# Optimization experiments

Measured on AMD Instinct MI355X. Metric: run time of the kernel, lower is better.

## Reference

```python
import jax, jax.numpy as jnp
import numpy as np

N, E = 20000, 320000
ATOM_IN, BOND_IN, HIDDEN, LAYERS = 64, 16, 256, 5
BN_EPS = 1e-5


def setup_inputs() -> dict:
    key = jax.random.key(0)
    ks = jax.random.split(key, 16)
    s = 0.05
    return {
        "x": jax.random.normal(ks[0], (N, ATOM_IN), jnp.float32),
        "edge_attr": jax.random.normal(ks[1], (E, BOND_IN), jnp.float32),
        "edge_index": jax.random.randint(ks[2], (2, E), 0, N, jnp.int32),
        "Wa": jax.random.normal(ks[3], (ATOM_IN, HIDDEN), jnp.float32) * s,
        "ba": jnp.zeros((HIDDEN,), jnp.float32),
        "We": jax.random.normal(ks[4], (BOND_IN, HIDDEN), jnp.float32) * s,
        "be": jnp.zeros((HIDDEN,), jnp.float32),
        "eps": jnp.zeros((LAYERS,), jnp.float32),  # train_eps=True, init 0
        "W1": jax.random.normal(ks[5], (LAYERS, HIDDEN, HIDDEN), jnp.float32) * s,
        "b1": jnp.zeros((LAYERS, HIDDEN), jnp.float32),
        "W2": jax.random.normal(ks[6], (LAYERS, HIDDEN, HIDDEN), jnp.float32) * s,
        "b2": jnp.zeros((LAYERS, HIDDEN), jnp.float32),
        "gamma": jnp.ones((LAYERS, HIDDEN), jnp.float32),
        "beta": jnp.zeros((LAYERS, HIDDEN), jnp.float32),
    }


def reference(x, edge_attr, edge_index, Wa, ba, We, be, eps, W1, b1, W2, b2, gamma, beta):
    src, dst = edge_index[0], edge_index[1]  # messages flow src -> dst (PyG x_j = x[src])
    h = x @ Wa + ba                          # [N, H] atom_proj
    e = edge_attr @ We + be                  # [E, H] edge_proj
    for l in range(LAYERS):
        # GINEConv: aggr = sum_j relu(x_j + e_ij); out = mlp((1+eps)*x_i + aggr)
        msg = jax.nn.relu(h[src] + e)                              # [E, H]
        aggr = jax.ops.segment_sum(msg, dst, num_segments=N)        # [N, H]
        z = (1.0 + eps[l]) * h + aggr
        z = jax.nn.relu(z @ W1[l] + b1[l]) @ W2[l] + b2[l]          # 2-layer MLP
        # BatchNorm1d over the node dimension (batch statistics)
        mu = jnp.mean(z, axis=0)
        var = jnp.var(z, axis=0)
        z = (z - mu) * jax.lax.rsqrt(var + BN_EPS) * gamma[l] + beta[l]
        z = jax.nn.relu(z)
        # dropout is identity in deterministic reference (eval)
        h = h + z  # residual
    return h
```

## Files before the change

kernel.cpp:

```cpp
#include <hip/hip_runtime.h>

typedef unsigned short u16;
typedef __attribute__((ext_vector_type(4))) float f32x4;
typedef __attribute__((ext_vector_type(8))) short s16x8;
typedef __attribute__((ext_vector_type(8))) unsigned short u16x8;
typedef __attribute__((ext_vector_type(4))) unsigned short u16x4;

__device__ inline float bf2f(u16 u) {
    unsigned v = ((unsigned)u) << 16;
    return __builtin_bit_cast(float, v);
}
__device__ inline u16 f2bf(float f) {
    unsigned u = __builtin_bit_cast(unsigned, f);
    unsigned r = (u + 0x7FFFu + ((u >> 16) & 1u)) >> 16;
    return (u16)r;
}

__global__ void count_kernel(const int* __restrict__ dst, int E, int* __restrict__ counts) {
    int e = blockIdx.x * 256 + threadIdx.x;
    if (e < E) atomicAdd(&counts[dst[e]], 1);
}

__global__ __launch_bounds__(1024) void scan_kernel(const int* __restrict__ counts,
    int* __restrict__ row_start, int* __restrict__ cursor, int NN) {
    __shared__ int sh[1024];
    const int tid = threadIdx.x;
    const int CH = (NN + 1023) / 1024;
    const int base = tid * CH;
    int sum = 0;
    for (int i = 0; i < CH; ++i) { int idx = base + i; if (idx < NN) sum += counts[idx]; }
    sh[tid] = sum; __syncthreads();
    for (int off = 1; off < 1024; off <<= 1) {
        int v = (tid >= off) ? sh[tid - off] : 0;
        __syncthreads();
        sh[tid] += v;
        __syncthreads();
    }
    int run = sh[tid] - sum;
    for (int i = 0; i < CH; ++i) {
        int idx = base + i;
        if (idx <= NN) {
            row_start[idx] = run;
            if (idx < NN) { cursor[idx] = run; run += counts[idx]; }
        }
    }
}

__global__ void pos_kernel(const int* __restrict__ src, const int* __restrict__ dst, int E,
    int* __restrict__ cursor, int* __restrict__ pos, int* __restrict__ src_perm) {
    int e = blockIdx.x * 256 + threadIdx.x;
    if (e < E) {
        int p = atomicAdd(&cursor[dst[e]], 1);
        pos[e] = p;
        src_perm[p] = src[e];
    }
}

__global__ void prep_kernel(const float* __restrict__ x, const float* __restrict__ Wa,
    const float* __restrict__ We, const float* __restrict__ W1, const float* __restrict__ W2,
    u16* __restrict__ x_bf, u16* __restrict__ Wat, u16* __restrict__ Wet,
    u16* __restrict__ W1t, u16* __restrict__ W2t, int NN) {
    int i = blockIdx.x * 256 + threadIdx.x;
    const int S0 = NN * 16;
    if (i < S0) {
        f32x4 v = *(const f32x4*)(x + (size_t)i * 4);
        u16x4 o; o.x = f2bf(v[0]); o.y = f2bf(v[1]); o.z = f2bf(v[2]); o.w = f2bf(v[3]);
        *(u16x4*)(x_bf + (size_t)i * 4) = o;
        return;
    }
    i -= S0;
    if (i < 16384) { int n = i >> 6, k = i & 63; Wat[i] = f2bf(Wa[k * 256 + n]); return; }
    i -= 16384;
    if (i < 8192) { int n = i >> 5, k = i & 31; Wet[i] = f2bf(k < 16 ? We[k * 256 + n] : 0.f); return; }
    i -= 8192;
    if (i < 327680) { int l = i >> 16, r = i & 65535, n = r >> 8, k = r & 255;
        W1t[i] = f2bf(W1[(size_t)l * 65536 + k * 256 + n]); return; }
    i -= 327680;
    if (i < 327680) { int l = i >> 16, r = i & 65535, n = r >> 8, k = r & 255;
        W2t[i] = f2bf(W2[(size_t)l * 65536 + k * 256 + n]); return; }
}

__global__ void permute_pad_eattr_kernel(const float* __restrict__ ea, const int* __restrict__ pos,
                                         int E, u16* __restrict__ out) {
    int e = blockIdx.x * 256 + threadIdx.x;
    if (e >= E) return;
    const float* r = ea + (size_t)e * 16;
    f32x4 q0 = *(const f32x4*)(r + 0);
    f32x4 q1 = *(const f32x4*)(r + 4);
    f32x4 q2 = *(const f32x4*)(r + 8);
    f32x4 q3 = *(const f32x4*)(r + 12);
    u16x8 v0, v1, z;
#pragma unroll
    for (int j = 0; j < 4; ++j) {
        v0[j] = f2bf(q0[j]); v0[4 + j] = f2bf(q1[j]);
        v1[j] = f2bf(q2[j]); v1[4 + j] = f2bf(q3[j]);
        z[j] = 0; z[4 + j] = 0;
    }
    u16* o = out + (size_t)pos[e] * 32;
    *(u16x8*)(o + 0) = v0;
    *(u16x8*)(o + 8) = v1;
    *(u16x8*)(o + 16) = z;
    *(u16x8*)(o + 24) = z;
}

template <bool WF32, bool WB16>
__global__ __launch_bounds__(256) void gemm_kernel(
    const u16* __restrict__ A, int lda, int M,
    const u16* __restrict__ Bt, int K,
    const float* __restrict__ bias,
    float* __restrict__ outF, u16* __restrict__ outB, int ldo) {
    __shared__ u16 As[128 * 32];
    __shared__ u16 Bs[128 * 32];
    const int tid = threadIdx.x, lane = tid & 63, wave = tid >> 6;
    const int m0 = blockIdx.x * 128, n0 = blockIdx.y * 128;
    const int wr = (wave >> 1) * 64, wc = (wave & 1) * 64;

    const f32x4 zero4 = {0.f, 0.f, 0.f, 0.f};
    f32x4 acc[4][4];
#pragma unroll
    for (int m = 0; m < 4; ++m)
#pragma unroll
        for (int n = 0; n < 4; ++n) acc[m][n] = zero4;

    for (int k0 = 0; k0 < K; k0 += 32) {
#pragma unroll
        for (int i = 0; i < 2; ++i) {
            int seg = i * 256 + tid;
            int row = seg >> 2, sk = seg & 3;
            int gr = m0 + row; gr = gr < M ? gr : M - 1;
            u16x8 va = *(const u16x8*)(A + (size_t)gr * lda + k0 + sk * 8);
            *(u16x8*)(&As[row * 32 + sk * 8]) = va;
            u16x8 vb = *(const u16x8*)(Bt + (size_t)(n0 + row) * K + k0 + sk * 8);
            *(u16x8*)(&Bs[row * 32 + sk * 8]) = vb;
        }
        __syncthreads();
        const int rsel = lane & 15, koff = (lane >> 4) * 8;
        s16x8 af[4], bf[4];
#pragma unroll
        for (int m = 0; m < 4; ++m) af[m] = *(const s16x8*)(&As[(wr + m * 16 + rsel) * 32 + koff]);
#pragma unroll
        for (int n = 0; n < 4; ++n) bf[n] = *(const s16x8*)(&Bs[(wc + n * 16 + rsel) * 32 + koff]);
#pragma unroll
        for (int m = 0; m < 4; ++m)
#pragma unroll
            for (int n = 0; n < 4; ++n)
                acc[m][n] = __builtin_amdgcn_mfma_f32_16x16x32_bf16(af[m], bf[n], acc[m][n], 0, 0, 0);
        __syncthreads();
    }

    const int cl = lane & 15, rq = lane >> 4;
#pragma unroll
    for (int n = 0; n < 4; ++n) {
        const int gcol = n0 + wc + n * 16 + cl;
        const float bv = bias[gcol];
#pragma unroll
        for (int m = 0; m < 4; ++m) {
#pragma unroll
            for (int j = 0; j < 4; ++j) {
                int grow = m0 + wr + m * 16 + rq * 4 + j;
                if (grow < M) {
                    float v = acc[m][n][j] + bv;
                    long orow = (long)grow;
                    if constexpr (WF32) outF[orow * ldo + gcol] = v;
                    if constexpr (WB16) outB[orow * ldo + gcol] = f2bf(v);
                }
            }
        }
    }
}

__global__ __launch_bounds__(256) void mlp_fused_kernel(
    const u16* __restrict__ z, int M,
    const u16* __restrict__ W1t, const float* __restrict__ b1,
    const u16* __restrict__ W2t, const float* __restrict__ b2,
    u16* __restrict__ y2,
    float* __restrict__ colsum, float* __restrict__ colsumsq) {
    __shared__ u16 As[64 * 32];
    __shared__ u16 Bs[256 * 32];
    __shared__ u16 Ys[64 * 260];
    const int tid = threadIdx.x, lane = tid & 63, wave = tid >> 6;
    const int m0 = blockIdx.x * 64;
    const int wc = wave * 64;
    const int rsel = lane & 15, koff = (lane >> 4) * 8;
    const int cl = lane & 15, rq = lane >> 4;

    const f32x4 zero4 = {0.f, 0.f, 0.f, 0.f};
    f32x4 acc[4][4];
#pragma unroll
    for (int m = 0; m < 4; ++m)
#pragma unroll
        for (int n = 0; n < 4; ++n) acc[m][n] = zero4;

    for (int k0 = 0; k0 < 256; k0 += 32) {
        {
            int row = tid >> 2, sk = tid & 3;
            int gr = m0 + row; gr = gr < M ? gr : M - 1;
            u16x8 va = *(const u16x8*)(z + (size_t)gr * 256 + k0 + sk * 8);
            *(u16x8*)(&As[row * 32 + sk * 8]) = va;
        }
#pragma unroll
        for (int i = 0; i < 4; ++i) {
            int seg = i * 256 + tid;
            int row = seg >> 2, sk = seg & 3;
            u16x8 vb = *(const u16x8*)(W1t + (size_t)row * 256 + k0 + sk * 8);
            *(u16x8*)(&Bs[row * 32 + sk * 8]) = vb;
        }
        __syncthreads();
        s16x8 af[4], bf[4];
#pragma unroll
        for (int m = 0; m < 4; ++m) af[m] = *(const s16x8*)(&As[(m * 16 + rsel) * 32 + koff]);
#pragma unroll
        for (int n = 0; n < 4; ++n) bf[n] = *(const s16x8*)(&Bs[(wc + n * 16 + rsel) * 32 + koff]);
#pragma unroll
        for (int m = 0; m < 4; ++m)
#pragma unroll
            for (int n = 0; n < 4; ++n)
                acc[m][n] = __builtin_amdgcn_mfma_f32_16x16x32_bf16(af[m], bf[n], acc[m][n], 0, 0, 0);
        __syncthreads();
    }
#pragma unroll
    for (int n = 0; n < 4; ++n) {
        const int gcol = wc + n * 16 + cl;
        const float bv = b1[gcol];
#pragma unroll
        for (int m = 0; m < 4; ++m) {
#pragma unroll
            for (int j = 0; j < 4; ++j) {
                int row = m * 16 + rq * 4 + j;
                float v = fmaxf(acc[m][n][j] + bv, 0.f);
                Ys[row * 260 + gcol] = f2bf(v);
            }
        }
        acc[0][n] = zero4; acc[1][n] = zero4; acc[2][n] = zero4; acc[3][n] = zero4;
    }

    for (int k0 = 0; k0 < 256; k0 += 32) {
#pragma unroll
        for (int i = 0; i < 4; ++i) {
            int seg = i * 256 + tid;
            int row = seg >> 2, sk = seg & 3;
            u16x8 vb = *(const u16x8*)(W2t + (size_t)row * 256 + k0 + sk * 8);
            *(u16x8*)(&Bs[row * 32 + sk * 8]) = vb;
        }
        __syncthreads();
        s16x8 af[4], bf[4];
#pragma unroll
        for (int m = 0; m < 4; ++m) af[m] = *(const s16x8*)(&Ys[(m * 16 + rsel) * 260 + k0 + koff]);
#pragma unroll
        for (int n = 0; n < 4; ++n) bf[n] = *(const s16x8*)(&Bs[(wc + n * 16 + rsel) * 32 + koff]);
#pragma unroll
        for (int m = 0; m < 4; ++m)
#pragma unroll
            for (int n = 0; n < 4; ++n)
                acc[m][n] = __builtin_amdgcn_mfma_f32_16x16x32_bf16(af[m], bf[n], acc[m][n], 0, 0, 0);
        __syncthreads();
    }
#pragma unroll
    for (int n = 0; n < 4; ++n) {
        const int gcol = wc + n * 16 + cl;
        const float bv = b2[gcol];
        float s = 0.f, ss = 0.f;
#pragma unroll
        for (int m = 0; m < 4; ++m) {
#pragma unroll
            for (int j = 0; j < 4; ++j) {
                int grow = m0 + m * 16 + rq * 4 + j;
                if (grow < M) {
                    float v = acc[m][n][j] + bv;
                    y2[(size_t)grow * 256 + gcol] = f2bf(v);
                    s += v; ss += v * v;
                }
            }
        }
        s += __shfl_down(s, 32); ss += __shfl_down(ss, 32);
        s += __shfl_down(s, 16); ss += __shfl_down(ss, 16);
        if (rq == 0) {
            atomicAdd(&colsum[gcol], s);
            atomicAdd(&colsumsq[gcol], ss);
        }
    }
}

__global__ __launch_bounds__(256) void agg_kernel(
    const int* __restrict__ row_start, const int* __restrict__ src_perm,
    const u16* __restrict__ e_perm, const u16* __restrict__ h_bf,
    const float* __restrict__ h, const float* __restrict__ eps, int layer,
    u16* __restrict__ z_bf, int NN) {
    const int node = blockIdx.x * 4 + (threadIdx.x >> 6);
    const int lane = threadIdx.x & 63;
    const int c0 = lane * 4;
    if (node >= NN) return;
    const int s0 = row_start[node], s1 = row_start[node + 1];
    float a0 = 0.f, a1 = 0.f, a2 = 0.f, a3 = 0.f;
    const u16* ep = e_perm + (size_t)s0 * 256 + c0;
    int k = s0;
    for (; k + 1 < s1; k += 2, ep += 512) {
        const int sa = src_perm[k];
        const int sb = src_perm[k + 1];
        u16x4 ha = *(const u16x4*)(h_bf + (size_t)sa * 256 + c0);
        u16x4 hb = *(const u16x4*)(h_bf + (size_t)sb * 256 + c0);
        u16x4 ea = *(const u16x4*)(ep);
        u16x4 eb = *(const u16x4*)(ep + 256);
        a0 += fmaxf(bf2f(ha.x) + bf2f(ea.x), 0.f);
        a1 += fmaxf(bf2f(ha.y) + bf2f(ea.y), 0.f);
        a2 += fmaxf(bf2f(ha.z) + bf2f(ea.z), 0.f);
        a3 += fmaxf(bf2f(ha.w) + bf2f(ea.w), 0.f);
        a0 += fmaxf(bf2f(hb.x) + bf2f(eb.x), 0.f);
        a1 += fmaxf(bf2f(hb.y) + bf2f(eb.y), 0.f);
        a2 += fmaxf(bf2f(hb.z) + bf2f(eb.z), 0.f);
        a3 += fmaxf(bf2f(hb.w) + bf2f(eb.w), 0.f);
    }
    if (k < s1) {
        const int sa = src_perm[k];
        u16x4 ha = *(const u16x4*)(h_bf + (size_t)sa * 256 + c0);
        u16x4 ea = *(const u16x4*)(ep);
        a0 += fmaxf(bf2f(ha.x) + bf2f(ea.x), 0.f);
        a1 += fmaxf(bf2f(ha.y) + bf2f(ea.y), 0.f);
        a2 += fmaxf(bf2f(ha.z) + bf2f(ea.z), 0.f);
        a3 += fmaxf(bf2f(ha.w) + bf2f(ea.w), 0.f);
    }
    const float c = 1.f + eps[layer];
    const f32x4 hr = *(const f32x4*)(h + (size_t)node * 256 + c0);
    u16x4 z;
    z.x = f2bf(c * hr[0] + a0); z.y = f2bf(c * hr[1] + a1);
    z.z = f2bf(c * hr[2] + a2); z.w = f2bf(c * hr[3] + a3);
    *(u16x4*)(z_bf + (size_t)node * 256 + c0) = z;
}

__global__ __launch_bounds__(256) void bn_res_kernel(
    const u16* __restrict__ y2, const float* __restrict__ colsum,
    const float* __restrict__ colsumsq, const float* __restrict__ gamma,
    const float* __restrict__ beta, const float* __restrict__ hin,
    float* __restrict__ hout, u16* __restrict__ h_bf, int write_bf,
    float invN, int total4) {
    const int i = blockIdx.x * 256 + threadIdx.x;
    if (i >= total4) return;
    const size_t base = (size_t)i * 4;
    const int c0 = (int)(base & 255);
    u16x4 yv = *(const u16x4*)(y2 + base);
    f32x4 hv = *(const f32x4*)(hin + base);
    u16 ys[4] = {yv.x, yv.y, yv.z, yv.w};
    f32x4 res;
#pragma unroll
    for (int j = 0; j < 4; ++j) {
        const int c = c0 + j;
        const float mu = colsum[c] * invN;
        const float var = colsumsq[c] * invN - mu * mu;
        const float sc = gamma[c] * rsqrtf(var + 1e-5f);
        const float sh = beta[c] - mu * sc;
        float v = bf2f(ys[j]) * sc + sh;
        v = fmaxf(v, 0.f);
        res[j] = hv[j] + v;
    }
    *(f32x4*)(hout + base) = res;
    if (write_bf) {
        u16x4 hb; hb.x = f2bf(res[0]); hb.y = f2bf(res[1]); hb.z = f2bf(res[2]); hb.w = f2bf(res[3]);
        *(u16x4*)(h_bf + base) = hb;
    }
}

extern "C" void kernel_launch(void* const* d_in, const int* in_sizes, int n_in,
                              void* d_out, int out_size, void* d_ws, size_t ws_size,
                              hipStream_t stream) {
    const float* x    = (const float*)d_in[0];
    const float* ea   = (const float*)d_in[1];
    const int*   ei   = (const int*)d_in[2];
    const float* Wa   = (const float*)d_in[3];
    const float* ba   = (const float*)d_in[4];
    const float* We   = (const float*)d_in[5];
    const float* be   = (const float*)d_in[6];
    const float* eps  = (const float*)d_in[7];
    const float* W1   = (const float*)d_in[8];
    const float* b1   = (const float*)d_in[9];
    const float* W2   = (const float*)d_in[10];
    const float* b2   = (const float*)d_in[11];
    const float* gamma= (const float*)d_in[12];
    const float* beta = (const float*)d_in[13];

    const int NN = in_sizes[0] / 64;
    const int EE = in_sizes[1] / 16;
    const int* src = ei;
    const int* dst = ei + EE;

    char* p = (char*)d_ws;
    auto alloc = [&](size_t bytes) -> char* {
        char* r = p;
        p += (bytes + 255) & ~(size_t)255;
        return r;
    };
    int*   counts   = (int*)alloc((size_t)(NN + 1) * 4);
    float* colsum   = (float*)alloc(5 * 256 * 4);
    float* colsumsq = (float*)alloc(5 * 256 * 4);
    size_t zbytes   = (size_t)(p - (char*)counts);
    int*   row_start= (int*)alloc((size_t)(NN + 1) * 4);
    int*   cursor   = (int*)alloc((size_t)NN * 4);
    int*   pos      = (int*)alloc((size_t)EE * 4);
    int*   src_perm = (int*)alloc((size_t)EE * 4);
    u16*   x_bf     = (u16*)alloc((size_t)NN * 64 * 2);
    u16*   Wat      = (u16*)alloc(256 * 64 * 2);
    u16*   Wet      = (u16*)alloc(256 * 32 * 2);
    u16*   W1t      = (u16*)alloc((size_t)5 * 65536 * 2);
    u16*   W2t      = (u16*)alloc((size_t)5 * 65536 * 2);
    u16*   eap_perm = (u16*)alloc((size_t)EE * 32 * 2);
    u16*   e_perm   = (u16*)alloc((size_t)EE * 256 * 2);
    float* h        = (float*)alloc((size_t)NN * 256 * 4);
    u16*   h_bf     = (u16*)alloc((size_t)NN * 256 * 2);
    u16*   z_bf     = (u16*)alloc((size_t)NN * 256 * 2);
    u16*   y2       = (u16*)alloc((size_t)NN * 256 * 2);

    hipMemsetAsync(counts, 0, zbytes, stream);

    const int eb = (EE + 255) / 256;
    count_kernel<<<eb, 256, 0, stream>>>(dst, EE, counts);
    scan_kernel<<<1, 1024, 0, stream>>>(counts, row_start, cursor, NN);
    pos_kernel<<<eb, 256, 0, stream>>>(src, dst, EE, cursor, pos, src_perm);

    const int prep_total = NN * 16 + 16384 + 8192 + 327680 + 327680;
    prep_kernel<<<(prep_total + 255) / 256, 256, 0, stream>>>(x, Wa, We, W1, W2, x_bf, Wat, Wet, W1t, W2t, NN);
    permute_pad_eattr_kernel<<<eb, 256, 0, stream>>>(ea, pos, EE, eap_perm);

    dim3 gh((NN + 127) / 128, 2);
    gemm_kernel<true, true><<<gh, 256, 0, stream>>>(
        x_bf, 64, NN, Wat, 64, ba, h, h_bf, 256);
    dim3 ge((EE + 127) / 128, 2);
    gemm_kernel<false, true><<<ge, 256, 0, stream>>>(
        eap_perm, 32, EE, Wet, 32, be, nullptr, e_perm, 256);

    const float invN = 1.f / (float)NN;
    const int nb4 = (NN * 64 + 255) / 256;
    const int mlp_blocks = (NN + 63) / 64;
    for (int l = 0; l < 5; ++l) {
        agg_kernel<<<(NN + 3) / 4, 256, 0, stream>>>(
            row_start, src_perm, e_perm, h_bf, h, eps, l, z_bf, NN);
        mlp_fused_kernel<<<mlp_blocks, 256, 0, stream>>>(
            z_bf, NN, W1t + (size_t)l * 65536, b1 + l * 256,
            W2t + (size_t)l * 65536, b2 + l * 256, y2,
            colsum + l * 256, colsumsq + l * 256);
        bn_res_kernel<<<nb4, 256, 0, stream>>>(
            y2, colsum + l * 256, colsumsq + l * 256, gamma + l * 256, beta + l * 256,
            h, (l == 4) ? (float*)d_out : h, h_bf, (l < 4) ? 1 : 0, invN, NN * 64);
    }
}
```

Measured before the change: 692.7 us.

## Coalesce GEMM epilogue stores via LDS staging and widen aggregation loads

The edge-projection GEMM and the fused MLP kernel now stage bf16 outputs in shared memory and write full 16-byte rows to global memory, replacing scattered 2-byte stores. The aggregation kernel now has each half-wave handle a separate edge with 8-channel (16-byte) loads, four edges per iteration, and combines the halves with a cross-lane shuffle. This targets store inefficiency in the large edge GEMM and adds memory-level parallelism to the gather. In exchange it uses extra LDS, adds a barrier, and does masked dummy loads for tail edges.

After: 621.5 us. 1.11x faster.

```diff
diff --git a/kernel.cpp b/kernel.cpp
--- a/kernel.cpp
+++ b/kernel.cpp
@@ -103,8 +103,7 @@
     *(u16x8*)(o + 24) = z;
 }
 
-template <bool WF32, bool WB16>
-__global__ __launch_bounds__(256) void gemm_kernel(
+__global__ __launch_bounds__(256) void gemm_h0_kernel(
     const u16* __restrict__ A, int lda, int M,
     const u16* __restrict__ Bt, int K,
     const float* __restrict__ bias,
@@ -160,11 +159,81 @@
                 int grow = m0 + wr + m * 16 + rq * 4 + j;
                 if (grow < M) {
                     float v = acc[m][n][j] + bv;
-                    long orow = (long)grow;
-                    if constexpr (WF32) outF[orow * ldo + gcol] = v;
-                    if constexpr (WB16) outB[orow * ldo + gcol] = f2bf(v);
+                    outF[(size_t)grow * ldo + gcol] = v;
+                    outB[(size_t)grow * ldo + gcol] = f2bf(v);
                 }
             }
+        }
+    }
+}
+
+__global__ __launch_bounds__(256) void gemm_coal_kernel(
+    const u16* __restrict__ A, int lda, int M,
+    const u16* __restrict__ Bt, int K,
+    const float* __restrict__ bias,
+    u16* __restrict__ outB, int ldo) {
+    __shared__ u16 As[128 * 32];
+    __shared__ u16 Bs[128 * 32];
+    __shared__ u16 Cs[128 * 136];
+    const int tid = threadIdx.x, lane = tid & 63, wave = tid >> 6;
+    const int m0 = blockIdx.x * 128, n0 = blockIdx.y * 128;
+    const int wr = (wave >> 1) * 64, wc = (wave & 1) * 64;
+
+    const f32x4 zero4 = {0.f, 0.f, 0.f, 0.f};
+    f32x4 acc[4][4];
+#pragma unroll
+    for (int m = 0; m < 4; ++m)
+#pragma unroll
+        for (int n = 0; n < 4; ++n) acc[m][n] = zero4;
+
+    for (int k0 = 0; k0 < K; k0 += 32) {
+#pragma unroll
+        for (int i = 0; i < 2; ++i) {
+            int seg = i * 256 + tid;
+            int row = seg >> 2, sk = seg & 3;
+            int gr = m0 + row; gr = gr < M ? gr : M - 1;
+            u16x8 va = *(const u16x8*)(A + (size_t)gr * lda + k0 + sk * 8);
+            *(u16x8*)(&As[row * 32 + sk * 8]) = va;
+            u16x8 vb = *(const u16x8*)(Bt + (size_t)(n0 + row) * K + k0 + sk * 8);
+            *(u16x8*)(&Bs[row * 32 + sk * 8]) = vb;
+        }
+        __syncthreads();
+        const int rsel = lane & 15, koff = (lane >> 4) * 8;
+        s16x8 af[4], bf[4];
+#pragma unroll
+        for (int m = 0; m < 4; ++m) af[m] = *(const s16x8*)(&As[(wr + m * 16 + rsel) * 32 + koff]);
+#pragma unroll
+        for (int n = 0; n < 4; ++n) bf[n] = *(const s16x8*)(&Bs[(wc + n * 16 + rsel) * 32 + koff]);
+#pragma unroll
+        for (int m = 0; m < 4; ++m)
+#pragma unroll
+            for (int n = 0; n < 4; ++n)
+                acc[m][n] = __builtin_amdgcn_mfma_f32_16x16x32_bf16(af[m], bf[n], acc[m][n], 0, 0, 0);
+        __syncthreads();
+    }
+
+    const int cl = lane & 15, rq = lane >> 4;
+#pragma unroll
+    for (int n = 0; n < 4; ++n) {
+        const int col = wc + n * 16 + cl;
+        const float bv = bias[n0 + col];
+#pragma unroll
+        for (int m = 0; m < 4; ++m) {
+#pragma unroll
+            for (int j = 0; j < 4; ++j) {
+                int row = wr + m * 16 + rq * 4 + j;
+                Cs[row * 136 + col] = f2bf(acc[m][n][j] + bv);
+            }
+        }
+    }
+    __syncthreads();
+    for (int r0 = 0; r0 < 128; r0 += 16) {
+        int row = r0 + (tid >> 4);
+        int gr = m0 + row;
+        int cc = (tid & 15) * 8;
+        if (gr < M) {
+            u16x8 v = *(u16x8*)(&Cs[row * 136 + cc]);
+            *(u16x8*)(outB + (size_t)gr * ldo + n0 + cc) = v;
         }
     }
 }
@@ -264,12 +333,10 @@
         for (int m = 0; m < 4; ++m) {
 #pragma unroll
             for (int j = 0; j < 4; ++j) {
-                int grow = m0 + m * 16 + rq * 4 + j;
-                if (grow < M) {
-                    float v = acc[m][n][j] + bv;
-                    y2[(size_t)grow * 256 + gcol] = f2bf(v);
-                    s += v; ss += v * v;
-                }
+                int row = m * 16 + rq * 4 + j;
+                float v = acc[m][n][j] + bv;
+                Ys[row * 260 + gcol] = f2bf(v);
+                if (m0 + row < M) { s += v; ss += v * v; }
             }
         }
         s += __shfl_down(s, 32); ss += __shfl_down(ss, 32);
@@ -278,6 +345,13 @@
             atomicAdd(&colsum[gcol], s);
             atomicAdd(&colsumsq[gcol], ss);
         }
+    }
+    __syncthreads();
+    for (int r0 = 0; r0 < 64; r0 += 8) {
+        int row = r0 + (tid >> 5);
+        int gr = m0 + row;
+        int cc = (tid & 31) * 8;
+        if (gr < M) *(u16x8*)(y2 + (size_t)gr * 256 + cc) = *(u16x8*)(&Ys[row * 260 + cc]);
     }
 }
 
@@ -288,43 +362,44 @@
     u16* __restrict__ z_bf, int NN) {
     const int node = blockIdx.x * 4 + (threadIdx.x >> 6);
     const int lane = threadIdx.x & 63;
-    const int c0 = lane * 4;
+    const int half = lane >> 5;
+    const int c0 = (lane & 31) * 8;
     if (node >= NN) return;
     const int s0 = row_start[node], s1 = row_start[node + 1];
-    float a0 = 0.f, a1 = 0.f, a2 = 0.f, a3 = 0.f;
-    const u16* ep = e_perm + (size_t)s0 * 256 + c0;
-    int k = s0;
-    for (; k + 1 < s1; k += 2, ep += 512) {
-        const int sa = src_perm[k];
-        const int sb = src_perm[k + 1];
-        u16x4 ha = *(const u16x4*)(h_bf + (size_t)sa * 256 + c0);
-        u16x4 hb = *(const u16x4*)(h_bf + (size_t)sb * 256 + c0);
-        u16x4 ea = *(const u16x4*)(ep);
-        u16x4 eb = *(const u16x4*)(ep + 256);
-        a0 += fmaxf(bf2f(ha.x) + bf2f(ea.x), 0.f);
-        a1 += fmaxf(bf2f(ha.y) + bf2f(ea.y), 0.f);
-        a2 += fmaxf(bf2f(ha.z) + bf2f(ea.z), 0.f);
-        a3 += fmaxf(bf2f(ha.w) + bf2f(ea.w), 0.f);
-        a0 += fmaxf(bf2f(hb.x) + bf2f(eb.x), 0.f);
-        a1 += fmaxf(bf2f(hb.y) + bf2f(eb.y), 0.f);
-        a2 += fmaxf(bf2f(hb.z) + bf2f(eb.z), 0.f);
-        a3 += fmaxf(bf2f(hb.w) + bf2f(eb.w), 0.f);
-    }
-    if (k < s1) {
-        const int sa = src_perm[k];
-        u16x4 ha = *(const u16x4*)(h_bf + (size_t)sa * 256 + c0);
-        u16x4 ea = *(const u16x4*)(ep);
-        a0 += fmaxf(bf2f(ha.x) + bf2f(ea.x), 0.f);
-        a1 += fmaxf(bf2f(ha.y) + bf2f(ea.y), 0.f);
-        a2 += fmaxf(bf2f(ha.z) + bf2f(ea.z), 0.f);
-        a3 += fmaxf(bf2f(ha.w) + bf2f(ea.w), 0.f);
-    }
-    const float c = 1.f + eps[layer];
-    const f32x4 hr = *(const f32x4*)(h + (size_t)node * 256 + c0);
-    u16x4 z;
-    z.x = f2bf(c * hr[0] + a0); z.y = f2bf(c * hr[1] + a1);
-    z.z = f2bf(c * hr[2] + a2); z.w = f2bf(c * hr[3] + a3);
-    *(u16x4*)(z_bf + (size_t)node * 256 + c0) = z;
+    float a[8] = {0.f, 0.f, 0.f, 0.f, 0.f, 0.f, 0.f, 0.f};
+    for (int k = s0; k < s1; k += 4) {
+        const int ke0 = k + half, ke1 = k + 2 + half;
+        const bool v0 = ke0 < s1, v1 = ke1 < s1;
+        const int i0 = v0 ? ke0 : s1 - 1;
+        const int i1 = v1 ? ke1 : s1 - 1;
+        const int su0 = src_perm[i0];
+        const int su1 = src_perm[i1];
+        u16x8 e0 = *(const u16x8*)(e_perm + (size_t)i0 * 256 + c0);
+        u16x8 h0 = *(const u16x8*)(h_bf + (size_t)su0 * 256 + c0);
+        u16x8 e1 = *(const u16x8*)(e_perm + (size_t)i1 * 256 + c0);
+        u16x8 h1 = *(const u16x8*)(h_bf + (size_t)su1 * 256 + c0);
+        const float m0 = v0 ? 1.f : 0.f;
+        const float m1 = v1 ? 1.f : 0.f;
+#pragma unroll
+        for (int j = 0; j < 8; ++j) {
+            a[j] += m0 * fmaxf(bf2f((u16)e0[j]) + bf2f((u16)h0[j]), 0.f);
+            a[j] += m1 * fmaxf(bf2f((u16)e1[j]) + bf2f((u16)h1[j]), 0.f);
+        }
+    }
+#pragma unroll
+    for (int j = 0; j < 8; ++j) a[j] += __shfl_xor(a[j], 32);
+    if (half == 0) {
+        const float c = 1.f + eps[layer];
+        const f32x4 hr0 = *(const f32x4*)(h + (size_t)node * 256 + c0);
+        const f32x4 hr1 = *(const f32x4*)(h + (size_t)node * 256 + c0 + 4);
+        u16x8 z;
+#pragma unroll
+        for (int j = 0; j < 4; ++j) {
+            z[j] = f2bf(c * hr0[j] + a[j]);
+            z[4 + j] = f2bf(c * hr1[j] + a[4 + j]);
+        }
+        *(u16x8*)(z_bf + (size_t)node * 256 + c0) = z;
+    }
 }
 
 __global__ __launch_bounds__(256) void bn_res_kernel(
@@ -420,11 +495,11 @@
     permute_pad_eattr_kernel<<<eb, 256, 0, stream>>>(ea, pos, EE, eap_perm);
 
     dim3 gh((NN + 127) / 128, 2);
-    gemm_kernel<true, true><<<gh, 256, 0, stream>>>(
+    gemm_h0_kernel<<<gh, 256, 0, stream>>>(
         x_bf, 64, NN, Wat, 64, ba, h, h_bf, 256);
     dim3 ge((EE + 127) / 128, 2);
-    gemm_kernel<false, true><<<ge, 256, 0, stream>>>(
-        eap_perm, 32, EE, Wet, 32, be, nullptr, e_perm, 256);
+    gemm_coal_kernel<<<ge, 256, 0, stream>>>(
+        eap_perm, 32, EE, Wet, 32, be, e_perm, 256);
 
     const float invN = 1.f / (float)NN;
     const int nb4 = (NN * 64 + 255) / 256;
```

## Recompute edge projection on the fly inside aggregation via MFMA instead of materializing

Applied to the files above, without the earlier changes.

Drops the precomputed E×256 bf16 edge-embedding buffer and its GEMM. The aggregation kernel now recomputes each edge's projection per layer with MFMA from the padded 32-wide edge attributes, with the bias folded in as a constant-1 column, and adds the gathered source node features. This removes a large per-layer read of edge embeddings and one write pass, at the cost of redundant MFMA compute each layer and a cross-lane reduction. The MLP epilogue is also changed to stage outputs through shared memory for coalesced vector stores.

Result: slower. 862.8 us (+24.6%).

```diff
diff --git a/kernel.cpp b/kernel.cpp
--- a/kernel.cpp
+++ b/kernel.cpp
@@ -57,7 +57,8 @@
 }
 
 __global__ void prep_kernel(const float* __restrict__ x, const float* __restrict__ Wa,
-    const float* __restrict__ We, const float* __restrict__ W1, const float* __restrict__ W2,
+    const float* __restrict__ We, const float* __restrict__ be,
+    const float* __restrict__ W1, const float* __restrict__ W2,
     u16* __restrict__ x_bf, u16* __restrict__ Wat, u16* __restrict__ Wet,
     u16* __restrict__ W1t, u16* __restrict__ W2t, int NN) {
     int i = blockIdx.x * 256 + threadIdx.x;
@@ -71,7 +72,11 @@
     i -= S0;
     if (i < 16384) { int n = i >> 6, k = i & 63; Wat[i] = f2bf(Wa[k * 256 + n]); return; }
     i -= 16384;
-    if (i < 8192) { int n = i >> 5, k = i & 31; Wet[i] = f2bf(k < 16 ? We[k * 256 + n] : 0.f); return; }
+    if (i < 8192) {
+        int n = i >> 5, k = i & 31;
+        float v = (k < 16) ? We[k * 256 + n] : ((k == 16) ? be[n] : 0.f);
+        Wet[i] = f2bf(v); return;
+    }
     i -= 8192;
     if (i < 327680) { int l = i >> 16, r = i & 65535, n = r >> 8, k = r & 255;
         W1t[i] = f2bf(W1[(size_t)l * 65536 + k * 256 + n]); return; }
@@ -89,22 +94,22 @@
     f32x4 q1 = *(const f32x4*)(r + 4);
     f32x4 q2 = *(const f32x4*)(r + 8);
     f32x4 q3 = *(const f32x4*)(r + 12);
-    u16x8 v0, v1, z;
+    u16x8 v0, v1, m, z;
 #pragma unroll
     for (int j = 0; j < 4; ++j) {
         v0[j] = f2bf(q0[j]); v0[4 + j] = f2bf(q1[j]);
         v1[j] = f2bf(q2[j]); v1[4 + j] = f2bf(q3[j]);
-        z[j] = 0; z[4 + j] = 0;
-    }
+        m[j] = 0; m[4 + j] = 0; z[j] = 0; z[4 + j] = 0;
+    }
+    m[0] = 0x3F80;
     u16* o = out + (size_t)pos[e] * 32;
     *(u16x8*)(o + 0) = v0;
     *(u16x8*)(o + 8) = v1;
-    *(u16x8*)(o + 16) = z;
+    *(u16x8*)(o + 16) = m;
     *(u16x8*)(o + 24) = z;
 }
 
-template <bool WF32, bool WB16>
-__global__ __launch_bounds__(256) void gemm_kernel(
+__global__ __launch_bounds__(256) void gemm_h0_kernel(
     const u16* __restrict__ A, int lda, int M,
     const u16* __restrict__ Bt, int K,
     const float* __restrict__ bias,
@@ -160,9 +165,8 @@
                 int grow = m0 + wr + m * 16 + rq * 4 + j;
                 if (grow < M) {
                     float v = acc[m][n][j] + bv;
-                    long orow = (long)grow;
-                    if constexpr (WF32) outF[orow * ldo + gcol] = v;
-                    if constexpr (WB16) outB[orow * ldo + gcol] = f2bf(v);
+                    outF[(size_t)grow * ldo + gcol] = v;
+                    outB[(size_t)grow * ldo + gcol] = f2bf(v);
                 }
             }
         }
@@ -264,12 +268,10 @@
         for (int m = 0; m < 4; ++m) {
 #pragma unroll
             for (int j = 0; j < 4; ++j) {
-                int grow = m0 + m * 16 + rq * 4 + j;
-                if (grow < M) {
-                    float v = acc[m][n][j] + bv;
-                    y2[(size_t)grow * 256 + gcol] = f2bf(v);
-                    s += v; ss += v * v;
-                }
+                int row = m * 16 + rq * 4 + j;
+                float v = acc[m][n][j] + bv;
+                Ys[row * 260 + gcol] = f2bf(v);
+                if (m0 + row < M) { s += v; ss += v * v; }
             }
         }
         s += __shfl_down(s, 32); ss += __shfl_down(ss, 32);
@@ -279,52 +281,88 @@
             atomicAdd(&colsumsq[gcol], ss);
         }
     }
-}
-
-__global__ __launch_bounds__(256) void agg_kernel(
+    __syncthreads();
+    for (int r0 = 0; r0 < 64; r0 += 8) {
+        int row = r0 + (tid >> 5);
+        int gr = m0 + row;
+        int cc = (tid & 31) * 8;
+        if (gr < M) *(u16x8*)(y2 + (size_t)gr * 256 + cc) = *(u16x8*)(&Ys[row * 260 + cc]);
+    }
+}
+
+__global__ __launch_bounds__(256) void agg_mfma_kernel(
     const int* __restrict__ row_start, const int* __restrict__ src_perm,
-    const u16* __restrict__ e_perm, const u16* __restrict__ h_bf,
-    const float* __restrict__ h, const float* __restrict__ eps, int layer,
+    const u16* __restrict__ eap, const u16* __restrict__ Wet,
+    const u16* __restrict__ h_bf, const float* __restrict__ h,
+    const float* __restrict__ eps, int layer,
     u16* __restrict__ z_bf, int NN) {
-    const int node = blockIdx.x * 4 + (threadIdx.x >> 6);
-    const int lane = threadIdx.x & 63;
-    const int c0 = lane * 4;
+    __shared__ u16 WetL[16 * 64 * 8];
+    const int tid = threadIdx.x;
+    const int lane = tid & 63;
+    const int rsel = lane & 15;
+    const int q = lane >> 4;
+#pragma unroll
+    for (int i = 0; i < 4; ++i) {
+        int ent = tid + i * 256;
+        int b = ent >> 6, l = ent & 63;
+        int row = b * 16 + (l & 15);
+        int ko = (l >> 4) * 8;
+        *(u16x8*)(&WetL[ent * 8]) = *(const u16x8*)(Wet + row * 32 + ko);
+    }
+    __syncthreads();
+
+    const int node = blockIdx.x * 4 + (tid >> 6);
     if (node >= NN) return;
     const int s0 = row_start[node], s1 = row_start[node + 1];
-    float a0 = 0.f, a1 = 0.f, a2 = 0.f, a3 = 0.f;
-    const u16* ep = e_perm + (size_t)s0 * 256 + c0;
-    int k = s0;
-    for (; k + 1 < s1; k += 2, ep += 512) {
-        const int sa = src_perm[k];
-        const int sb = src_perm[k + 1];
-        u16x4 ha = *(const u16x4*)(h_bf + (size_t)sa * 256 + c0);
-        u16x4 hb = *(const u16x4*)(h_bf + (size_t)sb * 256 + c0);
-        u16x4 ea = *(const u16x4*)(ep);
-        u16x4 eb = *(const u16x4*)(ep + 256);
-        a0 += fmaxf(bf2f(ha.x) + bf2f(ea.x), 0.f);
-        a1 += fmaxf(bf2f(ha.y) + bf2f(ea.y), 0.f);
-        a2 += fmaxf(bf2f(ha.z) + bf2f(ea.z), 0.f);
-        a3 += fmaxf(bf2f(ha.w) + bf2f(ea.w), 0.f);
-        a0 += fmaxf(bf2f(hb.x) + bf2f(eb.x), 0.f);
-        a1 += fmaxf(bf2f(hb.y) + bf2f(eb.y), 0.f);
-        a2 += fmaxf(bf2f(hb.z) + bf2f(eb.z), 0.f);
-        a3 += fmaxf(bf2f(hb.w) + bf2f(eb.w), 0.f);
-    }
-    if (k < s1) {
-        const int sa = src_perm[k];
-        u16x4 ha = *(const u16x4*)(h_bf + (size_t)sa * 256 + c0);
-        u16x4 ea = *(const u16x4*)(ep);
-        a0 += fmaxf(bf2f(ha.x) + bf2f(ea.x), 0.f);
-        a1 += fmaxf(bf2f(ha.y) + bf2f(ea.y), 0.f);
-        a2 += fmaxf(bf2f(ha.z) + bf2f(ea.z), 0.f);
-        a3 += fmaxf(bf2f(ha.w) + bf2f(ea.w), 0.f);
-    }
+
+    const f32x4 zero4 = {0.f, 0.f, 0.f, 0.f};
+    f32x4 sums[16];
+#pragma unroll
+    for (int b = 0; b < 16; ++b) sums[b] = zero4;
+
+    for (int e0 = s0; e0 < s1; e0 += 16) {
+        const int eidx = e0 + rsel;
+        const bool valid = eidx < s1;
+        const int ec = valid ? eidx : s1 - 1;
+        const int srcv = src_perm[ec];
+        s16x8 eaf = *(const s16x8*)(eap + (size_t)ec * 32 + q * 8);
+        const u16* hrow = h_bf + (size_t)srcv * 256 + q * 4;
+#pragma unroll
+        for (int b = 0; b < 16; ++b) {
+            s16x8 wf = *(const s16x8*)(&WetL[(b * 64 + lane) * 8]);
+            f32x4 d = __builtin_amdgcn_mfma_f32_16x16x32_bf16(wf, eaf, zero4, 0, 0, 0);
+            u16x4 hv = *(const u16x4*)(hrow + b * 16);
+#pragma unroll
+            for (int j = 0; j < 4; ++j) {
+                float t = fmaxf(d[j] + bf2f(hv[j]), 0.f);
+                sums[b][j] += valid ? t : 0.f;
+            }
+        }
+    }
+
+#pragma unroll
+    for (int b = 0; b < 16; ++b) {
+#pragma unroll
+        for (int j = 0; j < 4; ++j) {
+            float v = sums[b][j];
+            v += __shfl_xor(v, 1);
+            v += __shfl_xor(v, 2);
+            v += __shfl_xor(v, 4);
+            v += __shfl_xor(v, 8);
+            sums[b][j] = v;
+        }
+    }
+    f32x4 out = sums[0];
+#pragma unroll
+    for (int b = 1; b < 16; ++b) if (rsel == b) out = sums[b];
+
     const float c = 1.f + eps[layer];
-    const f32x4 hr = *(const f32x4*)(h + (size_t)node * 256 + c0);
+    const int col = rsel * 16 + q * 4;
+    const f32x4 hr = *(const f32x4*)(h + (size_t)node * 256 + col);
     u16x4 z;
-    z.x = f2bf(c * hr[0] + a0); z.y = f2bf(c * hr[1] + a1);
-    z.z = f2bf(c * hr[2] + a2); z.w = f2bf(c * hr[3] + a3);
-    *(u16x4*)(z_bf + (size_t)node * 256 + c0) = z;
+#pragma unroll
+    for (int j = 0; j < 4; ++j) z[j] = f2bf(c * hr[j] + out[j]);
+    *(u16x4*)(z_bf + (size_t)node * 256 + col) = z;
 }
 
 __global__ __launch_bounds__(256) void bn_res_kernel(
@@ -402,7 +440,6 @@
     u16*   W1t      = (u16*)alloc((size_t)5 * 65536 * 2);
     u16*   W2t      = (u16*)alloc((size_t)5 * 65536 * 2);
     u16*   eap_perm = (u16*)alloc((size_t)EE * 32 * 2);
-    u16*   e_perm   = (u16*)alloc((size_t)EE * 256 * 2);
     float* h        = (float*)alloc((size_t)NN * 256 * 4);
     u16*   h_bf     = (u16*)alloc((size_t)NN * 256 * 2);
     u16*   z_bf     = (u16*)alloc((size_t)NN * 256 * 2);
@@ -416,22 +453,20 @@
     pos_kernel<<<eb, 256, 0, stream>>>(src, dst, EE, cursor, pos, src_perm);
 
     const int prep_total = NN * 16 + 16384 + 8192 + 327680 + 327680;
-    prep_kernel<<<(prep_total + 255) / 256, 256, 0, stream>>>(x, Wa, We, W1, W2, x_bf, Wat, Wet, W1t, W2t, NN);
+    prep_kernel<<<(prep_total + 255) / 256, 256, 0, stream>>>(
+        x, Wa, We, be, W1, W2, x_bf, Wat, Wet, W1t, W2t, NN);
     permute_pad_eattr_kernel<<<eb, 256, 0, stream>>>(ea, pos, EE, eap_perm);
 
     dim3 gh((NN + 127) / 128, 2);
-    gemm_kernel<true, true><<<gh, 256, 0, stream>>>(
+    gemm_h0_kernel<<<gh, 256, 0, stream>>>(
         x_bf, 64, NN, Wat, 64, ba, h, h_bf, 256);
-    dim3 ge((EE + 127) / 128, 2);
-    gemm_kernel<false, true><<<ge, 256, 0, stream>>>(
-        eap_perm, 32, EE, Wet, 32, be, nullptr, e_perm, 256);
 
     const float invN = 1.f / (float)NN;
     const int nb4 = (NN * 64 + 255) / 256;
     const int mlp_blocks = (NN + 63) / 64;
     for (int l = 0; l < 5; ++l) {
-        agg_kernel<<<(NN + 3) / 4, 256, 0, stream>>>(
-            row_start, src_perm, e_perm, h_bf, h, eps, l, z_bf, NN);
+        agg_mfma_kernel<<<(NN + 3) / 4, 256, 0, stream>>>(
+            row_start, src_perm, eap_perm, Wet, h_bf, h, eps, l, z_bf, NN);
         mlp_fused_kernel<<<mlp_blocks, 256, 0, stream>>>(
             z_bf, NN, W1t + (size_t)l * 65536, b1 + l * 256,
             W2t + (size_t)l * 65536, b2 + l * 256, y2,
```
